# Kernel optimization log

Hardware: AMD Instinct MI355X
Metric: run time of the kernel (lower is better)

Reference implementation:

```python
import jax, jax.numpy as jnp
import numpy as np

D_MODEL = 2048
N_HEADS = 16
N_KV_HEADS = 4
HEAD_DIM = 128
ROPE_THETA = 10000.0


def _rope_cos_sin(T, hd, theta):
    # [T, hd//2]
    inv_freq = 1.0 / (theta ** (jnp.arange(0, hd, 2, dtype=jnp.float32) / hd))
    ang = jnp.arange(T, dtype=jnp.float32)[:, None] * inv_freq[None, :]
    return jnp.cos(ang), jnp.sin(ang)


def _apply_rope(x, cos, sin):
    # x: [B, H, T, hd]; rotate-half (Llama-style) RoPE
    hd = x.shape[-1]
    x1, x2 = x[..., : hd // 2], x[..., hd // 2 :]
    c = cos[None, None, :, :]
    s = sin[None, None, :, :]
    return jnp.concatenate([x1 * c - x2 * s, x2 * c + x1 * s], axis=-1)


def setup_inputs() -> dict:
    key = jax.random.key(0)
    ks = jax.random.split(key, 5)
    B, T = 2, 2048
    x = jax.random.normal(ks[0], (B, T, D_MODEL), dtype=jnp.float32)
    sq = 1.0 / np.sqrt(D_MODEL)
    Wq = jax.random.normal(ks[1], (D_MODEL, N_HEADS * HEAD_DIM), dtype=jnp.float32) * sq
    Wk = jax.random.normal(ks[2], (D_MODEL, N_KV_HEADS * HEAD_DIM), dtype=jnp.float32) * sq
    Wv = jax.random.normal(ks[3], (D_MODEL, N_KV_HEADS * HEAD_DIM), dtype=jnp.float32) * sq
    Wo = jax.random.normal(ks[4], (N_HEADS * HEAD_DIM, D_MODEL), dtype=jnp.float32) * sq
    return {"x": x, "Wq": Wq, "Wk": Wk, "Wv": Wv, "Wo": Wo}


def reference(x, Wq, Wk, Wv, Wo):
    B, T, _ = x.shape
    H, KV, hd = N_HEADS, N_KV_HEADS, HEAD_DIM
    n_rep = H // KV

    q = (x @ Wq).reshape(B, T, H, hd).transpose(0, 2, 1, 3)    # [B,H,T,hd]
    k = (x @ Wk).reshape(B, T, KV, hd).transpose(0, 2, 1, 3)   # [B,KV,T,hd]
    v = (x @ Wv).reshape(B, T, KV, hd).transpose(0, 2, 1, 3)

    cos, sin = _rope_cos_sin(T, hd, ROPE_THETA)
    q = _apply_rope(q, cos, sin)
    k = _apply_rope(k, cos, sin)

    # repeat KV heads for GQA: [B,KV,T,hd] -> [B,H,T,hd]
    k = jnp.repeat(k, n_rep, axis=1)
    v = jnp.repeat(v, n_rep, axis=1)

    scale = 1.0 / jnp.sqrt(jnp.float32(hd))
    scores = jnp.einsum("bhqd,bhkd->bhqk", q, k) * scale       # [B,H,T,T]
    causal = jnp.tril(jnp.ones((T, T), dtype=bool))
    scores = jnp.where(causal[None, None, :, :], scores, -jnp.inf)
    attn = jax.nn.softmax(scores, axis=-1)
    out = jnp.einsum("bhqk,bhkd->bhqd", attn, v)               # [B,H,T,hd]
    out = out.transpose(0, 2, 1, 3).reshape(B, T, H * hd)
    return out @ Wo
```

## Files before the change

### kernel.cpp

```cpp
#include <hip/hip_runtime.h>
#include <stdint.h>

#define T_SEQ 2048
#define DM    2048
#define NH    16
#define NKV   4
#define HD    128
#define MROWS 4096
#define NQKV  3072

typedef unsigned short u16;
typedef __bf16 bf16x8 __attribute__((ext_vector_type(8)));
typedef float  f32x4  __attribute__((ext_vector_type(4)));

__device__ __forceinline__ u16 f2b(float f) {
  union { float f; unsigned u; } v; v.f = f;
  return (u16)((v.u + 0x7fffu + ((v.u >> 16) & 1u)) >> 16);
}
__device__ __forceinline__ float b2f(u16 u) {
  union { unsigned u; float f; } v; v.u = ((unsigned)u) << 16;
  return v.f;
}
__device__ __forceinline__ void gl_lds16(const u16* g, u16* l) {
  __builtin_amdgcn_global_load_lds(
      (__attribute__((address_space(1))) void*)g,
      (__attribute__((address_space(3))) void*)l, 16, 0, 0);
}
__device__ __forceinline__ void storev(float* p, float v) { *p = v; }
__device__ __forceinline__ void storev(u16* p, float v)   { *p = f2b(v); }

__global__ __launch_bounds__(256) void k_cvt_x(const float* __restrict__ x,
                                               u16* __restrict__ o, int n) {
  int i = (blockIdx.x * 256 + threadIdx.x) * 4;
  if (i >= n) return;
  float4 v = *(const float4*)(x + i);
  ushort4 r;
  r.x = f2b(v.x); r.y = f2b(v.y); r.z = f2b(v.z); r.w = f2b(v.w);
  *(ushort4*)(o + i) = r;
}

__global__ __launch_bounds__(256) void k_tw4(const float* __restrict__ Wq,
                                             const float* __restrict__ Wk,
                                             const float* __restrict__ Wv,
                                             const float* __restrict__ Wo,
                                             u16* __restrict__ WT,
                                             u16* __restrict__ Wot) {
  __shared__ float tl[32][33];
  int z = blockIdx.z;
  const float* in; u16* out; int Nd, xt;
  if (z < 64)      { in = Wq; out = WT;               Nd = 2048; xt = z; }
  else if (z < 80) { in = Wk; out = WT + 2048 * 2048; Nd = 512;  xt = z - 64; }
  else if (z < 96) { in = Wv; out = WT + 2560 * 2048; Nd = 512;  xt = z - 80; }
  else             { in = Wo; out = Wot;              Nd = 2048; xt = z - 96; }
  int n0 = xt * 32, k0 = blockIdx.y * 32;
  int tx = threadIdx.x, ty = threadIdx.y;
#pragma unroll
  for (int i = 0; i < 32; i += 8)
    tl[ty + i][tx] = in[(long)(k0 + ty + i) * Nd + n0 + tx];
  __syncthreads();
#pragma unroll
  for (int i = 0; i < 32; i += 8)
    out[(long)(n0 + ty + i) * 2048 + k0 + tx] = f2b(tl[tx][ty + i]);
}

template <int BN, typename OutT>
__global__ __launch_bounds__(512, 2) void k_gemm8(const u16* __restrict__ A,
                                                  const u16* __restrict__ Bt,
                                                  OutT* __restrict__ C,
                                                  int M, int N, int K) {
  constexpr int NJ = BN / 128;
  constexpr int BH = NJ;
  __shared__ __align__(16) u16 As[2][256 * 64];
  __shared__ __align__(16) u16 Bs[2][BN * 64];
  const int tid = threadIdx.x;
  const int wv = tid >> 6, lane = tid & 63;
  const int quad = lane >> 4, ln = lane & 15, ln7 = lane & 7 & 7;
  const int wm = wv & 1, wn = wv >> 1;
  const long m0 = (long)blockIdx.x * 256;
  const long n0 = (long)blockIdx.y * BN;
  const int so = wv << 1;
  const int lr8 = lane >> 3;
  const int gch = (lane & 7) ^ lr8;

  f32x4 acc[8][2 * NJ] = {};
  bf16x8 Af[4][2], Bf[2 * NJ][2];

  auto stage = [&](const u16* __restrict__ G, long grow0, long kcol, u16* lds) {
#pragma unroll
    for (int o = 0; o < 2; ++o) {
      int lr = (so + o) * 8;
      gl_lds16(G + (grow0 + lr + lr8) * (long)K + kcol + gch * 8, lds + lr * 64);
    }
  };

#define READ_A(MH)                                                            \
  _Pragma("unroll") for (int i = 0; i < 4; ++i)                               \
      _Pragma("unroll") for (int s = 0; s < 2; ++s)                           \
          Af[i][s] = *(const bf16x8*)&asc[((MH)*64 + i * 16 + ln) * 64 +      \
                                          (((s * 4 + quad) ^ (ln & 7)) << 3)];
#define READ_B(NHq)                                                           \
  _Pragma("unroll") for (int jj = 0; jj < NJ; ++jj)                           \
      _Pragma("unroll") for (int s = 0; s < 2; ++s)                           \
          Bf[(NHq)*NJ + jj][s] =                                              \
              *(const bf16x8*)&bsc[(((NHq)*NJ + jj) * 16 + ln) * 64 +         \
                                   (((s * 4 + quad) ^ (ln & 7)) << 3)];
#define MMA_Q(MH, NHq)                                                        \
  _Pragma("unroll") for (int i = 0; i < 4; ++i)                               \
      _Pragma("unroll") for (int jj = 0; jj < NJ; ++jj) {                     \
        acc[(MH)*4 + i][(NHq)*NJ + jj] =                                      \
            __builtin_amdgcn_mfma_f32_16x16x32_bf16(                          \
                Af[i][0], Bf[(NHq)*NJ + jj][0],                               \
                acc[(MH)*4 + i][(NHq)*NJ + jj], 0, 0, 0);                     \
        acc[(MH)*4 + i][(NHq)*NJ + jj] =                                      \
            __builtin_amdgcn_mfma_f32_16x16x32_bf16(                          \
                Af[i][1], Bf[(NHq)*NJ + jj][1],                               \
                acc[(MH)*4 + i][(NHq)*NJ + jj], 0, 0, 0);                     \
      }
#define PH_MID()                                                              \
  __builtin_amdgcn_s_barrier();                                               \
  asm volatile("s_waitcnt lgkmcnt(0)" ::: "memory");                          \
  __builtin_amdgcn_s_setprio(1)
#define PH_END()                                                              \
  __builtin_amdgcn_s_setprio(0);                                              \
  __builtin_amdgcn_s_barrier()

  const int NT = K >> 6;
  stage(Bt, n0, 0, Bs[0]);
  if (BH == 2) stage(Bt, n0 + 128, 0, Bs[0] + 128 * 64);
  stage(A, m0, 0, As[0]);
  stage(A, m0 + 128, 0, As[0] + 128 * 64);
  stage(Bt, n0, 64, Bs[1]);
  if (BH == 2) stage(Bt, n0 + 128, 64, Bs[1] + 128 * 64);
  asm volatile("s_waitcnt vmcnt(%0)" ::"i"(2 * BH) : "memory");
  __builtin_amdgcn_s_barrier();

  for (int t = 0; t < NT; ++t) {
    const int par = t & 1;
    const u16* asc = As[par] + wm * (128 * 64);
    const u16* bsc = Bs[par] + wn * (32 * NJ * 64);
    u16* an = As[par ^ 1];
    u16* bp = Bs[par];
    const bool pa = (t + 1 < NT), pb = (t + 2 < NT);
    if (pa) stage(A, m0, (long)(t + 1) * 64, an);
    READ_A(0); READ_B(0);
    PH_MID(); MMA_Q(0, 0); PH_END();
    if (pa) stage(A, m0 + 128, (long)(t + 1) * 64, an + 128 * 64);
    READ_B(1);
    PH_MID(); MMA_Q(0, 1); PH_END();
    if (pb) stage(Bt, n0, (long)(t + 2) * 64, bp);
    READ_A(1);
    PH_MID(); MMA_Q(1, 1); PH_END();
    if (BH == 2 && pb) stage(Bt, n0 + 128, (long)(t + 2) * 64, bp + 128 * 64);
    if (pb) asm volatile("s_waitcnt vmcnt(%0)" ::"i"(2 * BH) : "memory");
    else    asm volatile("s_waitcnt vmcnt(0)" ::: "memory");
    PH_MID(); MMA_Q(1, 0); PH_END();
  }
#undef READ_A
#undef READ_B
#undef MMA_Q
#undef PH_MID
#undef PH_END
  (void)ln7;
#pragma unroll
  for (int i = 0; i < 8; ++i) {
    long row = m0 + wm * 128 + i * 16 + quad * 4;
#pragma unroll
    for (int j = 0; j < 2 * NJ; ++j) {
      long col = n0 + wn * (32 * NJ) + j * 16 + ln;
#pragma unroll
      for (int r = 0; r < 4; ++r)
        storev(&C[(row + r) * N + col], acc[i][j][r]);
    }
  }
}

__global__ __launch_bounds__(256) void k_rope2(const u16* __restrict__ C,
                                               u16* __restrict__ Qo,
                                               u16* __restrict__ Ko) {
  int idx = blockIdx.x * 256 + threadIdx.x;
  int d = idx & 63;
  int t = (idx >> 6) & (T_SEQ - 1);
  int g = idx >> 17;
  int b = (g >= 20) ? 1 : 0;
  int hh = g - b * 20;
  int isQ = hh < 16;
  int head = isQ ? hh : (hh - 16);
  int coloff = isQ ? 0 : 2048;
  float qscale = isQ ? 0.12751745f : 1.0f;
  u16* o = isQ ? Qo : Ko;
  int nh = isQ ? NH : NKV;
  long inb = (long)(b * T_SEQ + t) * NQKV + coloff + head * HD + d;
  float q1 = b2f(C[inb]);
  float q2 = b2f(C[inb + 64]);
  float inv = __expf(-0.14391156f * (float)d);
  float sn, cs;
  __sincosf((float)t * inv, &sn, &cs);
  long ob = (((long)b * nh + head) * T_SEQ + t) * HD + d;
  o[ob]      = f2b((q1 * cs - q2 * sn) * qscale);
  o[ob + 64] = f2b((q2 * cs + q1 * sn) * qscale);
}

__global__ __launch_bounds__(256) void k_vt(const u16* __restrict__ C,
                                            u16* __restrict__ Vt) {
  __shared__ u16 tl[32][33];
  int bkv = blockIdx.z;
  int t0 = blockIdx.x * 32, d0 = blockIdx.y * 32;
  int tx = threadIdx.x, ty = threadIdx.y;
  int b = bkv >> 2, kv = bkv & 3;
#pragma unroll
  for (int i = 0; i < 32; i += 8)
    tl[ty + i][tx] = C[(long)(b * T_SEQ + t0 + ty + i) * NQKV + 2560 + kv * HD + d0 + tx];
  __syncthreads();
#pragma unroll
  for (int i = 0; i < 32; i += 8)
    Vt[((long)bkv * HD + d0 + ty + i) * T_SEQ + t0 + tx] = tl[tx][ty + i];
}

template <bool DIAG>
__device__ __forceinline__ void p_emit(f32x4 (&S)[4], u16* __restrict__ Pb,
                                       int quad, int ln, int mrow) {
#pragma unroll
  for (int nt = 0; nt < 4; ++nt)
#pragma unroll
    for (int r = 0; r < 4; ++r) {
      float v = S[nt][r];
      if (DIAG) v = (nt * 16 + ln <= mrow + r) ? v : -1e30f;
      float pv = exp2f(v - 8.0f);
      int row = quad * 4 + r;
      int chnk = (nt * 2 + (ln >> 3)) ^ (row & 7);
      *(__bf16*)&Pb[row * 64 + chnk * 8 + (ln & 7)] = (__bf16)pv;
    }
}

__global__ __launch_bounds__(256, 2) void k_attn(const u16* __restrict__ Q,
                                                 const u16* __restrict__ Kg,
                                                 const u16* __restrict__ Vt,
                                                 u16* __restrict__ Og) {
  __shared__ __align__(16) u16 Ks[64 * 128];
  __shared__ __align__(16) u16 Vs[128 * 64];
  __shared__ __align__(16) u16 Ps[4][2][16 * 64];
  const int tid = threadIdx.x;
  const int wv = tid >> 6, lane = tid & 63;
  const int quad = lane >> 4, ln = lane & 15;
  const int bh = blockIdx.y;
  const int b = bh >> 4, h = bh & 15;
  const int kvh = h >> 2;
  const int p = blockIdx.x;
  const int thi = 31 - p, tlo = p;
  const int qhi = thi * 64 + wv * 16;
  const int qlo = tlo * 64 + wv * 16;

  bf16x8 qfh[4], qfl[4];
  {
    const u16* qp = Q + ((long)bh * T_SEQ + qhi + ln) * HD + quad * 8;
#pragma unroll
    for (int s = 0; s < 4; ++s) qfh[s] = *(const bf16x8*)(qp + s * 32);
    qp = Q + ((long)bh * T_SEQ + qlo + ln) * HD + quad * 8;
#pragma unroll
    for (int s = 0; s < 4; ++s) qfl[s] = *(const bf16x8*)(qp + s * 32);
  }
  bf16x8 onesb;
#pragma unroll
  for (int i = 0; i < 8; ++i) onesb[i] = (__bf16)1.0f;

  f32x4 lh = {0.f, 0.f, 0.f, 0.f}, ll = {0.f, 0.f, 0.f, 0.f};
  f32x4 oh[8] = {}, ol[8] = {};

  const u16* Kb = Kg + (long)(b * NKV + kvh) * T_SEQ * HD;
  const u16* Vb = Vt + (long)(b * NKV + kvh) * HD * T_SEQ;

  for (int kt = 0; kt <= thi; ++kt) {
    const int k0 = kt * 64;
#pragma unroll
    for (int r = 0; r < 4; ++r) {
      int s = r * 256 + tid;
      gl_lds16(Kb + (long)(k0 + (s >> 4)) * HD + (((s & 15) ^ ((s >> 4) & 15)) << 3),
               &Ks[(r * 256 + wv * 64) * 8]);
      gl_lds16(Vb + (long)(s >> 3) * T_SEQ + k0 + (((s & 7) ^ ((s >> 3) & 7)) << 3),
               &Vs[(r * 256 + wv * 64) * 8]);
    }
    __syncthreads();
    const bool lo_act = (kt <= tlo);
    f32x4 Sh[4], Sl[4];
#pragma unroll
    for (int nt = 0; nt < 4; ++nt) {
      bf16x8 kb[4];
      const u16* kp = &Ks[(nt * 16 + ln) * 128];
#pragma unroll
      for (int ss = 0; ss < 4; ++ss)
        kb[ss] = *(const bf16x8*)(kp + (((quad + 4 * ss) ^ ln) << 3));
      f32x4 s = {0.f, 0.f, 0.f, 0.f};
#pragma unroll
      for (int ss = 0; ss < 4; ++ss)
        s = __builtin_amdgcn_mfma_f32_16x16x32_bf16(qfh[ss], kb[ss], s, 0, 0, 0);
      Sh[nt] = s;
      if (lo_act) {
        f32x4 t = {0.f, 0.f, 0.f, 0.f};
#pragma unroll
        for (int ss = 0; ss < 4; ++ss)
          t = __builtin_amdgcn_mfma_f32_16x16x32_bf16(qfl[ss], kb[ss], t, 0, 0, 0);
        Sl[nt] = t;
      }
    }
    if (kt == thi) p_emit<true>(Sh, &Ps[wv][0][0], quad, ln, wv * 16 + quad * 4);
    else           p_emit<false>(Sh, &Ps[wv][0][0], quad, ln, 0);
    if (lo_act) {
      if (kt == tlo) p_emit<true>(Sl, &Ps[wv][1][0], quad, ln, wv * 16 + quad * 4);
      else           p_emit<false>(Sl, &Ps[wv][1][0], quad, ln, 0);
    }
    asm volatile("s_waitcnt lgkmcnt(0)" ::: "memory");
    bf16x8 pfh[2], pfl[2];
#pragma unroll
    for (int ss = 0; ss < 2; ++ss)
      pfh[ss] = *(const bf16x8*)&Ps[wv][0][ln * 64 + (((ss * 4 + quad) ^ (ln & 7)) << 3)];
    if (lo_act) {
#pragma unroll
      for (int ss = 0; ss < 2; ++ss)
        pfl[ss] = *(const bf16x8*)&Ps[wv][1][ln * 64 + (((ss * 4 + quad) ^ (ln & 7)) << 3)];
    }
    lh = __builtin_amdgcn_mfma_f32_16x16x32_bf16(pfh[0], onesb, lh, 0, 0, 0);
    lh = __builtin_amdgcn_mfma_f32_16x16x32_bf16(pfh[1], onesb, lh, 0, 0, 0);
    if (lo_act) {
      ll = __builtin_amdgcn_mfma_f32_16x16x32_bf16(pfl[0], onesb, ll, 0, 0, 0);
      ll = __builtin_amdgcn_mfma_f32_16x16x32_bf16(pfl[1], onesb, ll, 0, 0, 0);
    }
#pragma unroll
    for (int dt = 0; dt < 8; ++dt) {
      bf16x8 vb[2];
      const u16* vp = &Vs[(dt * 16 + ln) * 64];
#pragma unroll
      for (int ss = 0; ss < 2; ++ss)
        vb[ss] = *(const bf16x8*)(vp + (((quad + 4 * ss) ^ (ln & 7)) << 3));
#pragma unroll
      for (int ss = 0; ss < 2; ++ss)
        oh[dt] = __builtin_amdgcn_mfma_f32_16x16x32_bf16(pfh[ss], vb[ss], oh[dt], 0, 0, 0);
      if (lo_act) {
#pragma unroll
        for (int ss = 0; ss < 2; ++ss)
          ol[dt] = __builtin_amdgcn_mfma_f32_16x16x32_bf16(pfl[ss], vb[ss], ol[dt], 0, 0, 0);
      }
    }
    __syncthreads();
  }
  float rh[4], rl[4];
#pragma unroll
  for (int r = 0; r < 4; ++r) { rh[r] = 1.f / lh[r]; rl[r] = 1.f / ll[r]; }
#pragma unroll
  for (int dt = 0; dt < 8; ++dt)
#pragma unroll
    for (int r = 0; r < 4; ++r) {
      long rowh = (long)b * T_SEQ + qhi + quad * 4 + r;
      long rowl = (long)b * T_SEQ + qlo + quad * 4 + r;
      Og[rowh * (NH * HD) + h * HD + dt * 16 + ln] = f2b(oh[dt][r] * rh[r]);
      Og[rowl * (NH * HD) + h * HD + dt * 16 + ln] = f2b(ol[dt][r] * rl[r]);
    }
}

extern "C" void kernel_launch(void* const* d_in, const int* in_sizes, int n_in,
                              void* d_out, int out_size, void* d_ws, size_t ws_size,
                              hipStream_t stream) {
  const float* x  = (const float*)d_in[0];
  const float* Wq = (const float*)d_in[1];
  const float* Wk = (const float*)d_in[2];
  const float* Wv = (const float*)d_in[3];
  const float* Wo = (const float*)d_in[4];
  float* out = (float*)d_out;
  char* ws = (char*)d_ws;
  u16* WT  = (u16*)(ws + 0);
  u16* Wot = (u16*)(ws + 12582912);
  u16* Cq  = (u16*)(ws + 20971520);
  u16* Xb  = (u16*)(ws + 46137344);
  u16* Kb  = (u16*)(ws + 62914560);
  u16* Vtb = (u16*)(ws + 67108864);
  u16* Qb = Xb;
  u16* attn = Cq;

  k_cvt_x<<<8192, 256, 0, stream>>>(x, Xb, MROWS * DM);
  k_tw4<<<dim3(1, 64, 160), dim3(32, 8), 0, stream>>>(Wq, Wk, Wv, Wo, WT, Wot);

  k_gemm8<256, u16><<<dim3(16, 12), 512, 0, stream>>>(Xb, WT, Cq, MROWS, NQKV, DM);

  k_rope2<<<20480, 256, 0, stream>>>(Cq, Qb, Kb);
  k_vt<<<dim3(64, 4, 8), dim3(32, 8), 0, stream>>>(Cq, Vtb);

  k_attn<<<dim3(16, 32), 256, 0, stream>>>(Qb, Kb, Vtb, attn);

  k_gemm8<128, float><<<dim3(16, 16), 512, 0, stream>>>(attn, Wot, out, MROWS, DM, 2048);
}
```

Baseline: 333.0 us.

## Specialize GEMM prefetch schedule per tile width: depth-2 for BN=256, fewer phases for BN=128

The GEMM main loop is split by tile width. For BN=256, both A and B tiles are now prefetched two iterations ahead into the same buffer being consumed, with stage issues placed after the reads of that half. For BN=128, the four MMA phases are merged into two barrier-separated phases, with A prefetched one step ahead and B two steps ahead. The aim is to hide more global-load latency and cut barrier overhead, at the risk of LDS read/write hazards if the waitcnt and barrier placement is not exact.

Result: faster. 310.3 us (-6.8%).

```diff
diff --git a/kernel.cpp b/kernel.cpp
--- a/kernel.cpp
+++ b/kernel.cpp
@@ -69,12 +69,11 @@
                                                   OutT* __restrict__ C,
                                                   int M, int N, int K) {
   constexpr int NJ = BN / 128;
-  constexpr int BH = NJ;
   __shared__ __align__(16) u16 As[2][256 * 64];
   __shared__ __align__(16) u16 Bs[2][BN * 64];
   const int tid = threadIdx.x;
   const int wv = tid >> 6, lane = tid & 63;
-  const int quad = lane >> 4, ln = lane & 15, ln7 = lane & 7 & 7;
+  const int quad = lane >> 4, ln = lane & 15;
   const int wm = wv & 1, wn = wv >> 1;
   const long m0 = (long)blockIdx.x * 256;
   const long n0 = (long)blockIdx.y * BN;
@@ -125,42 +124,64 @@
   __builtin_amdgcn_s_barrier()
 
   const int NT = K >> 6;
-  stage(Bt, n0, 0, Bs[0]);
-  if (BH == 2) stage(Bt, n0 + 128, 0, Bs[0] + 128 * 64);
-  stage(A, m0, 0, As[0]);
-  stage(A, m0 + 128, 0, As[0] + 128 * 64);
-  stage(Bt, n0, 64, Bs[1]);
-  if (BH == 2) stage(Bt, n0 + 128, 64, Bs[1] + 128 * 64);
-  asm volatile("s_waitcnt vmcnt(%0)" ::"i"(2 * BH) : "memory");
-  __builtin_amdgcn_s_barrier();
-
-  for (int t = 0; t < NT; ++t) {
-    const int par = t & 1;
-    const u16* asc = As[par] + wm * (128 * 64);
-    const u16* bsc = Bs[par] + wn * (32 * NJ * 64);
-    u16* an = As[par ^ 1];
-    u16* bp = Bs[par];
-    const bool pa = (t + 1 < NT), pb = (t + 2 < NT);
-    if (pa) stage(A, m0, (long)(t + 1) * 64, an);
-    READ_A(0); READ_B(0);
-    PH_MID(); MMA_Q(0, 0); PH_END();
-    if (pa) stage(A, m0 + 128, (long)(t + 1) * 64, an + 128 * 64);
-    READ_B(1);
-    PH_MID(); MMA_Q(0, 1); PH_END();
-    if (pb) stage(Bt, n0, (long)(t + 2) * 64, bp);
-    READ_A(1);
-    PH_MID(); MMA_Q(1, 1); PH_END();
-    if (BH == 2 && pb) stage(Bt, n0 + 128, (long)(t + 2) * 64, bp + 128 * 64);
-    if (pb) asm volatile("s_waitcnt vmcnt(%0)" ::"i"(2 * BH) : "memory");
-    else    asm volatile("s_waitcnt vmcnt(0)" ::: "memory");
-    PH_MID(); MMA_Q(1, 0); PH_END();
+  if constexpr (NJ == 2) {
+    stage(Bt, n0, 0, Bs[0]); stage(Bt, n0 + 128, 0, Bs[0] + 128 * 64);
+    stage(A,  m0, 0, As[0]); stage(A,  m0 + 128, 0, As[0] + 128 * 64);
+    stage(Bt, n0, 64, Bs[1]); stage(Bt, n0 + 128, 64, Bs[1] + 128 * 64);
+    stage(A,  m0, 64, As[1]); stage(A,  m0 + 128, 64, As[1] + 128 * 64);
+    asm volatile("s_waitcnt vmcnt(8)" ::: "memory");
+    __builtin_amdgcn_s_barrier();
+
+    for (int t = 0; t < NT; ++t) {
+      const int par = t & 1;
+      const u16* asc = As[par] + wm * (128 * 64);
+      const u16* bsc = Bs[par] + wn * (32 * NJ * 64);
+      u16* sa = As[par];
+      u16* sb = Bs[par];
+      const bool pf = (t + 2 < NT);
+      const long kc2 = (long)(t + 2) * 64;
+      READ_A(0); READ_B(0);
+      PH_MID(); MMA_Q(0, 0); PH_END();
+      READ_B(1);
+      PH_MID(); MMA_Q(0, 1); PH_END();
+      if (pf) { stage(Bt, n0, kc2, sb); stage(Bt, n0 + 128, kc2, sb + 128 * 64); }
+      READ_A(1);
+      PH_MID(); MMA_Q(1, 1); PH_END();
+      if (pf) { stage(A, m0, kc2, sa); stage(A, m0 + 128, kc2, sa + 128 * 64); }
+      if (pf) asm volatile("s_waitcnt vmcnt(8)" ::: "memory");
+      else    asm volatile("s_waitcnt vmcnt(0)" ::: "memory");
+      PH_MID(); MMA_Q(1, 0); PH_END();
+    }
+  } else {
+    stage(A,  m0, 0, As[0]); stage(A, m0 + 128, 0, As[0] + 128 * 64);
+    stage(Bt, n0, 0, Bs[0]);
+    stage(Bt, n0, 64, Bs[1]);
+    asm volatile("s_waitcnt vmcnt(2)" ::: "memory");
+    __builtin_amdgcn_s_barrier();
+
+    for (int t = 0; t < NT; ++t) {
+      const int par = t & 1;
+      const u16* asc = As[par] + wm * (128 * 64);
+      const u16* bsc = Bs[par] + wn * (32 * NJ * 64);
+      const bool pa = (t + 1 < NT), pb = (t + 2 < NT);
+      if (pa) {
+        stage(A, m0,       (long)(t + 1) * 64, As[par ^ 1]);
+        stage(A, m0 + 128, (long)(t + 1) * 64, As[par ^ 1] + 128 * 64);
+      }
+      READ_A(0); READ_B(0); READ_B(1);
+      PH_MID(); MMA_Q(0, 0); MMA_Q(0, 1); PH_END();
+      if (pb) stage(Bt, n0, (long)(t + 2) * 64, Bs[par]);
+      READ_A(1);
+      if (pb) asm volatile("s_waitcnt vmcnt(2)" ::: "memory");
+      else    asm volatile("s_waitcnt vmcnt(0)" ::: "memory");
+      PH_MID(); MMA_Q(1, 0); MMA_Q(1, 1); PH_END();
+    }
   }
 #undef READ_A
 #undef READ_B
 #undef MMA_Q
 #undef PH_MID
 #undef PH_END
-  (void)ln7;
 #pragma unroll
   for (int i = 0; i < 8; ++i) {
     long row = m0 + wm * 128 + i * 16 + quad * 4;
```
